# Performance work log

Hardware: AMD Instinct MI355X
Metric: run time of the kernel (lower is better)

## Reference

```python
import jax, jax.numpy as jnp
import numpy as np

N = 100000   # total nodes in batch
E = 400000   # directed edges (before self-loops)
G = 4000     # graphs in batch (~25 atoms/mol)
IN = 29; HID = 128; HEADS = 4
BN_EPS = 1e-5


def setup_inputs():
    ks = jax.random.split(jax.random.key(0), 64)
    def rn(i, shp, s=0.1):
        return jax.random.normal(ks[i], shp, dtype=jnp.float32) * s
    H4 = HEADS * HID
    inp = {
        "x": jax.random.normal(ks[0], (N, IN), dtype=jnp.float32),
        "edge_index": jax.random.randint(ks[1], (2, E), 0, N),
        "batch_idx": jnp.sort(jax.random.randint(ks[2], (N,), 0, G)),
        "context": jax.random.uniform(ks[3], (N, 9), dtype=jnp.float32),
        "props": jax.random.normal(ks[4], (G, 9), dtype=jnp.float32),
        "mask": jax.random.randint(ks[5], (N,), 0, 2).astype(bool),
        "W1": rn(6, (IN, H4)), "as1": rn(7, (HEADS, HID)), "ad1": rn(8, (HEADS, HID)), "b1": rn(9, (H4,)),
        "g1": jnp.ones((H4,)), "be1": jnp.zeros((H4,)), "rm1": rn(10, (H4,), 0.05),
        "rv1": jax.random.uniform(ks[11], (H4,), minval=0.5, maxval=1.5),
        "W2": rn(12, (H4, H4), 0.05), "as2": rn(13, (HEADS, HID)), "ad2": rn(14, (HEADS, HID)), "b2": rn(15, (H4,)),
        "g2": jnp.ones((H4,)), "be2": jnp.zeros((H4,)), "rm2": rn(16, (H4,), 0.05),
        "rv2": jax.random.uniform(ks[17], (H4,), minval=0.5, maxval=1.5),
        "W3": rn(18, (H4, HID), 0.05), "as3": rn(19, (1, HID)), "ad3": rn(20, (1, HID)), "b3": rn(21, (HID,)),
        "g3": jnp.ones((HID,)), "be3": jnp.zeros((HID,)), "rm3": rn(22, (HID,), 0.05),
        "rv3": jax.random.uniform(ks[23], (HID,), minval=0.5, maxval=1.5),
        # context head 128 -> 128 -> 9
        "cw1": rn(24, (HID, HID)), "cb1": jnp.zeros((HID,)), "cw2": rn(25, (HID, 9)), "cb2": jnp.zeros((9,)),
        # property head 128 -> 128 -> 9
        "pw1": rn(26, (HID, HID)), "pb1": jnp.zeros((HID,)), "pw2": rn(27, (HID, 9)), "pb2": jnp.zeros((9,)),
        # masked reconstruction head 128 -> 128 -> 29
        "mw1": rn(28, (HID, HID)), "mb1": jnp.zeros((HID,)), "mw2": rn(29, (HID, IN)), "mb2": jnp.zeros((IN,)),
    }
    return inp


def gat_layer(h_in, src, dst, n, W, a_src, a_dst, bias):
    """PyG GATConv (concat=True, negative_slope=0.2, self-loops already in src/dst)."""
    heads, C = a_src.shape
    h = (h_in @ W).reshape(n, heads, C)                       # [N, H, C]
    e = jax.nn.leaky_relu((h * a_src).sum(-1)[src] + (h * a_dst).sum(-1)[dst], 0.2)  # [E', H]
    m = jax.ops.segment_max(e, dst, num_segments=n)            # segment softmax over incoming edges
    p = jnp.exp(e - m[dst])
    denom = jax.ops.segment_sum(p, dst, num_segments=n)
    alpha = p / (denom[dst] + 1e-16)                           # [E', H]
    out = jax.ops.segment_sum(alpha[:, :, None] * h[src], dst, num_segments=n)  # [N, H, C]
    return out.reshape(n, heads * C) + bias


def bn_elu(x, g, b, rm, rv):
    # BatchNorm1d (eval mode: running stats) followed by ELU; dropout is identity in eval.
    return jax.nn.elu((x - rm) * (g / jnp.sqrt(rv + BN_EPS)) + b)


def reference(x, edge_index, batch_idx, context, props, mask,
              W1, as1, ad1, b1, g1, be1, rm1, rv1,
              W2, as2, ad2, b2, g2, be2, rm2, rv2,
              W3, as3, ad3, b3, g3, be3, rm3, rv3,
              cw1, cb1, cw2, cb2, pw1, pb1, pw2, pb2, mw1, mb1, mw2, mb2):
    n = x.shape[0]
    loop = jnp.arange(n)
    src = jnp.concatenate([edge_index[0], loop])  # PyG GATConv adds self-loops by default
    dst = jnp.concatenate([edge_index[1], loop])
    h = bn_elu(gat_layer(x, src, dst, n, W1, as1, ad1, b1), g1, be1, rm1, rv1)
    h = bn_elu(gat_layer(h, src, dst, n, W2, as2, ad2, b2), g2, be2, rm2, rv2)
    h = bn_elu(gat_layer(h, src, dst, n, W3, as3, ad3, b3), g3, be3, rm3, rv3)  # [N, 128]
    # global mean pool per graph
    cnt = jax.ops.segment_sum(jnp.ones((n,), h.dtype), batch_idx, num_segments=G)
    gemb = jax.ops.segment_sum(h, batch_idx, num_segments=G) / jnp.maximum(cnt, 1.0)[:, None]
    # context prediction (BCE with logits, mean)
    z = jax.nn.relu(h @ cw1 + cb1) @ cw2 + cb2
    context_loss = jnp.mean(jnp.logaddexp(0.0, z) - z * context)
    # property prediction (MSE, mean)
    pz = jax.nn.relu(gemb @ pw1 + pb1) @ pw2 + pb2
    property_loss = jnp.mean((pz - props) ** 2)
    # masked feature reconstruction: MSE over masked nodes (masked mean == mse on h[mask])
    mz = jax.nn.relu(h @ mw1 + mb1) @ mw2 + mb2
    mf = mask.astype(h.dtype)
    mask_loss = jnp.sum(mf[:, None] * (mz - x) ** 2) / (jnp.sum(mf) * x.shape[1])
    return context_loss + property_loss + 0.5 * mask_loss
```

## Files before the change

### kernel.cpp

```cpp
#include <hip/hip_runtime.h>
#include <hip/hip_bf16.h>
#include <cstdint>
#include <cstddef>
#include <type_traits>

#define HIDC 128

typedef __attribute__((ext_vector_type(8))) short short8v;
typedef __attribute__((ext_vector_type(4))) float float4v;

__device__ __forceinline__ float loadT(const float* p){ return *p; }
__device__ __forceinline__ float loadT(const __hip_bfloat16* p){ return __bfloat162float(*p); }
__device__ __forceinline__ void  storeT(float* p, float v){ *p = v; }
__device__ __forceinline__ void  storeT(__hip_bfloat16* p, float v){ *p = __float2bfloat16(v); }

__device__ __forceinline__ short f2bf(float f){
  __hip_bfloat16 h = __float2bfloat16(f);
  return *reinterpret_cast<short*>(&h);
}
__device__ __forceinline__ float bfbits2f(short s){
  return __uint_as_float(((unsigned)(unsigned short)s) << 16);
}

__device__ __forceinline__ int swz(int row, int k){ return (row*32 + k) ^ ((row & 7) << 3); }

template<typename TA, typename TC, bool BIAS, bool RELU>
__global__ __launch_bounds__(256)
void mfma_gemm_kernel(const TA* __restrict__ A, const float* __restrict__ B,
                      const float* __restrict__ bias, TC* __restrict__ C,
                      int M, int Nb, int K, int ldc)
{
  __shared__ short As[128*32];
  __shared__ short Bs[64*32];

  const int nwg = gridDim.x * gridDim.y;
  int orig = blockIdx.y * gridDim.x + blockIdx.x;
  int xcd = orig & 7, pos = orig >> 3;
  int q = nwg >> 3, r = nwg & 7;
  int logical = (xcd < r ? xcd*(q+1) : r*(q+1) + (xcd - r)*q) + pos;
  const int bx = logical % gridDim.x;
  const int by = logical / gridDim.x;

  const int tid  = threadIdx.x;
  const int brow = by * 128;
  const int bcol = bx * 64;
  const int lane = tid & 63;
  const int wave = tid >> 6;
  const int wm = (wave >> 1) * 64;
  const int wn = (wave & 1) * 32;
  const int l15 = lane & 15;
  const int kq  = lane >> 4;

  float4v acc[4][2];
  #pragma unroll
  for (int i = 0; i < 4; i++)
    #pragma unroll
    for (int j = 0; j < 2; j++)
      #pragma unroll
      for (int r2 = 0; r2 < 4; r2++) acc[i][j][r2] = 0.f;

  const int am  = tid >> 1;
  const int akb = (tid & 1) * 16;
  const int bn  = tid & 63;
  const int bkc = tid >> 6;

  const bool dma_ok = std::is_same<TA, __hip_bfloat16>::value &&
                      ((K & 31) == 0) && (brow + 128 <= M);
  int dma_r[2], dma_c[2];
  #pragma unroll
  for (int i = 0; i < 2; i++) {
    int j = (wave*2 + i)*64 + lane;
    int s2 = (j>>2)&1, s3 = (j>>3)&1, s4 = (j>>4)&1;
    int b2 = s2 ^ s4;
    int b1 = ((j>>1)&1) ^ s3;
    int b0 = (j&1) ^ b2;
    int src = (j & ~7) | (b2<<2) | (b1<<1) | b0;
    dma_r[i] = src >> 2;
    dma_c[i] = src & 3;
  }

  for (int k0 = 0; k0 < K; k0 += 32) {
    if (dma_ok) {
      const short* Ash = reinterpret_cast<const short*>(A);
      #pragma unroll
      for (int i = 0; i < 2; i++) {
        const short* gp = Ash + (size_t)(brow + dma_r[i])*K + k0 + dma_c[i]*8;
        __builtin_amdgcn_global_load_lds(
            (const __attribute__((address_space(1))) void*)gp,
            (__attribute__((address_space(3))) void*)&As[(wave*2 + i)*512],
            16, 0, 0);
      }
    } else {
      const int gm = brow + am;
      short s[16];
      if constexpr (std::is_same<TA, __hip_bfloat16>::value) {
        if (gm < M && (k0 + akb + 16) <= K) {
          const short8v* p = reinterpret_cast<const short8v*>(
              reinterpret_cast<const short*>(A) + (size_t)gm*K + k0 + akb);
          short8v v0 = p[0];
          *(short8v*)&As[swz(am, akb)]     = v0;
          short8v v1 = p[1];
          *(short8v*)&As[swz(am, akb + 8)] = v1;
          goto a_done;
        }
      }
      #pragma unroll
      for (int j = 0; j < 16; j++) {
        int gk = k0 + akb + j;
        s[j] = (gm < M && gk < K) ? f2bf(loadT(&A[(size_t)gm*K + gk])) : (short)0;
      }
      {
        short8v v0, v1;
        #pragma unroll
        for (int j = 0; j < 8; j++) { v0[j] = s[j]; v1[j] = s[j+8]; }
        *(short8v*)&As[swz(am, akb)]     = v0;
        *(short8v*)&As[swz(am, akb + 8)] = v1;
      }
      a_done:;
    }
    {
      const int gcol = bcol + bn;
      short8v v;
      #pragma unroll
      for (int j = 0; j < 8; j++) {
        int gk = k0 + bkc*8 + j;
        v[j] = (gk < K && gcol < Nb) ? f2bf(B[(size_t)gk*Nb + gcol]) : (short)0;
      }
      *(short8v*)&Bs[swz(bn, bkc*8)] = v;
    }
    __syncthreads();

    short8v bfrag[2];
    #pragma unroll
    for (int ni = 0; ni < 2; ni++)
      bfrag[ni] = *(const short8v*)&Bs[swz(wn + ni*16 + l15, kq*8)];
    #pragma unroll
    for (int mi = 0; mi < 4; mi++) {
      short8v afrag = *(const short8v*)&As[swz(wm + mi*16 + l15, kq*8)];
      #pragma unroll
      for (int ni = 0; ni < 2; ni++)
        acc[mi][ni] = __builtin_amdgcn_mfma_f32_16x16x32_bf16(afrag, bfrag[ni], acc[mi][ni], 0, 0, 0);
    }
    __syncthreads();
  }

  #pragma unroll
  for (int mi = 0; mi < 4; mi++) {
    #pragma unroll
    for (int r2 = 0; r2 < 4; r2++) {
      int row = brow + wm + mi*16 + kq*4 + r2;
      if (row >= M) continue;
      #pragma unroll
      for (int ni = 0; ni < 2; ni++) {
        int col = bcol + wn + ni*16 + l15;
        if (col >= Nb) continue;
        float v = acc[mi][ni][r2];
        if (BIAS) v += bias[col];
        if (RELU) v = fmaxf(v, 0.f);
        storeT(&C[(size_t)row*ldc + col], v);
      }
    }
  }
}

template<typename T>
__global__ void scores_kernel(const T* __restrict__ hW, const float* __restrict__ a_src,
                              const float* __restrict__ a_dst, float* __restrict__ s_src,
                              float* __restrict__ s_dst, int n, int H)
{
  const int lane = threadIdx.x & 63;
  const int wid = blockIdx.x*(blockDim.x>>6) + (threadIdx.x>>6);
  if (wid >= n*H) return;
  const int node = wid / H, h = wid % H;
  const T* row = hW + (size_t)node*H*HIDC + (size_t)h*HIDC;
  float ss = 0.f, sd = 0.f;
  for (int c = lane; c < HIDC; c += 64) {
    float v = loadT(&row[c]);
    ss += v * a_src[h*HIDC + c];
    sd += v * a_dst[h*HIDC + c];
  }
  #pragma unroll
  for (int off = 32; off; off >>= 1) {
    ss += __shfl_down(ss, off);
    sd += __shfl_down(sd, off);
  }
  if (lane == 0) { s_src[wid] = ss; s_dst[wid] = sd; }
}

__global__ void deg_count_kernel(const int* __restrict__ ei, int E, int EP, int* __restrict__ deg)
{
  int e = blockIdx.x*blockDim.x + threadIdx.x;
  if (e >= EP) return;
  int d = (e < E) ? ei[E + e] : (e - E);
  atomicAdd(&deg[d], 1);
}

__global__ __launch_bounds__(256)
void scan1_kernel(const int* __restrict__ deg, int* __restrict__ indptr,
                  int* __restrict__ bsum, int n)
{
  __shared__ int sh[256];
  const int b = blockIdx.x, t = threadIdx.x;
  const int base = b*1024 + t*4;
  int v0 = (base+0 < n) ? deg[base+0] : 0;
  int v1 = (base+1 < n) ? deg[base+1] : 0;
  int v2 = (base+2 < n) ? deg[base+2] : 0;
  int v3 = (base+3 < n) ? deg[base+3] : 0;
  int tsum = v0+v1+v2+v3;
  sh[t] = tsum;
  __syncthreads();
  for (int off = 1; off < 256; off <<= 1) {
    int x = (t >= off) ? sh[t-off] : 0;
    __syncthreads();
    sh[t] += x;
    __syncthreads();
  }
  int run = sh[t] - tsum;
  if (base+0 < n) indptr[base+0] = run; run += v0;
  if (base+1 < n) indptr[base+1] = run; run += v1;
  if (base+2 < n) indptr[base+2] = run; run += v2;
  if (base+3 < n) indptr[base+3] = run;
  if (t == 255) bsum[b] = sh[255];
}

__global__ void scan2_kernel(int* __restrict__ bsum, int B)
{
  if (blockIdx.x == 0 && threadIdx.x == 0) {
    int run = 0;
    for (int i = 0; i < B; i++) { int v = bsum[i]; bsum[i] = run; run += v; }
  }
}

__global__ void scan3_kernel(int* __restrict__ indptr, const int* __restrict__ bsum,
                             int n, int total)
{
  int i = blockIdx.x*blockDim.x + threadIdx.x;
  if (i < n) indptr[i] += bsum[i >> 10];
  if (i == 0) indptr[n] = total;
}

__global__ void fill_kernel(const int* __restrict__ ei, int E, int EP,
                            const int* __restrict__ indptr, int* __restrict__ ctr,
                            int* __restrict__ esrc)
{
  int e = blockIdx.x*blockDim.x + threadIdx.x;
  if (e >= EP) return;
  int s, d;
  if (e < E) { s = ei[e]; d = ei[E + e]; } else { s = d = e - E; }
  int pos = indptr[d] + atomicAdd(&ctr[d], 1);
  esrc[pos] = s;
}

typedef __hip_bfloat16 bf16;

template<int H>
__global__ void csr_attn_agg_kernel(const int* __restrict__ indptr, const int* __restrict__ esrc,
                                    const float* __restrict__ s_src, const float* __restrict__ s_dst,
                                    const bf16* __restrict__ hW, bf16* __restrict__ out, int n,
                                    const float* __restrict__ bias, const float* __restrict__ g,
                                    const float* __restrict__ be, const float* __restrict__ rm,
                                    const float* __restrict__ rv)
{
  constexpr int HD = H * HIDC;
  const int lane = threadIdx.x & 63;
  const int wid = blockIdx.x*(blockDim.x>>6) + (threadIdx.x>>6);
  if (wid >= n*H) return;
  const int dst = wid / H, h = wid - dst*H;
  const int beg = indptr[dst], end = indptr[dst+1];
  const int deg = end - beg;
  const float sdh = s_dst[dst*H + h];

  float acc0 = 0.f, acc1 = 0.f;

  if (deg <= 64) {
    int sk = (lane < deg) ? esrc[beg + lane] : -1;
    float sc = -3.0e38f;
    if (sk >= 0) {
      float v = s_src[(size_t)sk*H + h] + sdh;
      sc = (v >= 0.f) ? v : 0.2f*v;
    }
    float m = sc;
    #pragma unroll
    for (int off = 32; off; off >>= 1) m = fmaxf(m, __shfl_xor(m, off));
    float e = (sk >= 0) ? __expf(sc - m) : 0.f;
    float den = e;
    #pragma unroll
    for (int off = 32; off; off >>= 1) den += __shfl_xor(den, off);
    const float rden = 1.f / (den + 1e-16f);
    for (int k = 0; k < deg; ++k) {
      float a = __shfl(e, k) * rden;
      int s = __shfl(sk, k);
      const bf16* row = hW + (size_t)s*HD + h*HIDC;
      acc0 += a * loadT(&row[lane]);
      acc1 += a * loadT(&row[lane + 64]);
    }
  } else {
    float m = -3.0e38f;
    for (int k = beg + lane; k < end; k += 64) {
      float v = s_src[(size_t)esrc[k]*H + h] + sdh;
      v = (v >= 0.f) ? v : 0.2f*v;
      m = fmaxf(m, v);
    }
    #pragma unroll
    for (int off = 32; off; off >>= 1) m = fmaxf(m, __shfl_xor(m, off));
    float den = 0.f;
    for (int k = beg + lane; k < end; k += 64) {
      float v = s_src[(size_t)esrc[k]*H + h] + sdh;
      v = (v >= 0.f) ? v : 0.2f*v;
      den += __expf(v - m);
    }
    #pragma unroll
    for (int off = 32; off; off >>= 1) den += __shfl_xor(den, off);
    const float rden = 1.f / (den + 1e-16f);
    for (int k = beg; k < end; ++k) {
      int s = esrc[k];
      float v = s_src[(size_t)s*H + h] + sdh;
      v = (v >= 0.f) ? v : 0.2f*v;
      float a = __expf(v - m) * rden;
      const bf16* row = hW + (size_t)s*HD + h*HIDC;
      acc0 += a * loadT(&row[lane]);
      acc1 += a * loadT(&row[lane + 64]);
    }
  }

  const int c0 = h*HIDC + lane;
  const int c1 = c0 + 64;
  float y0 = (acc0 + bias[c0] - rm[c0]) * (g[c0] / sqrtf(rv[c0] + 1e-5f)) + be[c0];
  float y1 = (acc1 + bias[c1] - rm[c1]) * (g[c1] / sqrtf(rv[c1] + 1e-5f)) + be[c1];
  y0 = (y0 > 0.f) ? y0 : expm1f(y0);
  y1 = (y1 > 0.f) ? y1 : expm1f(y1);
  bf16* orow = out + (size_t)dst*HD + h*HIDC;
  storeT(&orow[lane], y0);
  storeT(&orow[lane + 64], y1);
}

template<typename T>
__global__ void pool_sum_kernel(const T* __restrict__ h, const int* __restrict__ batch,
                                float* __restrict__ gsum, float* __restrict__ cnt, int n)
{
  int idx = blockIdx.x*blockDim.x + threadIdx.x;
  if (idx >= n*HIDC) return;
  int node = idx >> 7, j = idx & 127;
  int g = batch[node];
  atomicAdd(&gsum[(size_t)g*HIDC + j], loadT(&h[idx]));
  if (j == 0) atomicAdd(&cnt[g], 1.f);
}

__global__ void pool_div_kernel(float* __restrict__ gsum, const float* __restrict__ cnt, int G)
{
  int idx = blockIdx.x*blockDim.x + threadIdx.x;
  if (idx >= G*HIDC) return;
  gsum[idx] /= fmaxf(cnt[idx >> 7], 1.f);
}

__global__ void mask_detect_kernel(const int* __restrict__ m, int nwords, int* __restrict__ flag)
{
  int i = blockIdx.x*blockDim.x + threadIdx.x;
  if (i >= nwords) return;
  unsigned v = (unsigned)m[i];
  if (v > 1u) atomicOr(flag, 1);
}

__global__ __launch_bounds__(256)
void bce_reduce_kernel(const float* __restrict__ z, const float* __restrict__ ctx,
                       float* __restrict__ out_sum, int n)
{
  __shared__ float sh[256];
  float local = 0.f;
  const long long total = (long long)n * 9;
  for (long long i = (long long)blockIdx.x*blockDim.x + threadIdx.x; i < total;
       i += (long long)gridDim.x*blockDim.x) {
    int row = (int)(i / 9), j = (int)(i - (long long)row*9);
    float zz = z[(size_t)row*32 + j];
    float la = fmaxf(zz, 0.f) + log1pf(expf(-fabsf(zz)));
    local += la - zz * ctx[i];
  }
  sh[threadIdx.x] = local;
  __syncthreads();
  for (int s = 128; s; s >>= 1) {
    if ((int)threadIdx.x < s) sh[threadIdx.x] += sh[threadIdx.x + s];
    __syncthreads();
  }
  if (threadIdx.x == 0) atomicAdd(out_sum, sh[0]);
}

__global__ __launch_bounds__(256)
void mse_mask_reduce_kernel(const float* __restrict__ z, const float* __restrict__ x,
                            const int* __restrict__ mask, const int* __restrict__ bytemode,
                            float* __restrict__ out_sum, float* __restrict__ out_cnt, int n)
{
  __shared__ float sh[256], sh2[256];
  float local = 0.f, cl = 0.f;
  const bool bm = (*bytemode) != 0;
  const long long total = (long long)n * 29;
  for (long long i = (long long)blockIdx.x*blockDim.x + threadIdx.x; i < total;
       i += (long long)gridDim.x*blockDim.x) {
    int row = (int)(i / 29), j = (int)(i - (long long)row*29);
    int mk = bm ? (int)((const unsigned char*)mask)[row] : mask[row];
    if (mk != 0) {
      float dd = z[(size_t)row*32 + j] - x[i];
      local += dd*dd;
      if (j == 0) cl += 1.f;
    }
  }
  sh[threadIdx.x] = local;
  sh2[threadIdx.x] = cl;
  __syncthreads();
  for (int s = 128; s; s >>= 1) {
    if ((int)threadIdx.x < s) { sh[threadIdx.x] += sh[threadIdx.x + s]; sh2[threadIdx.x] += sh2[threadIdx.x + s]; }
    __syncthreads();
  }
  if (threadIdx.x == 0) { atomicAdd(out_sum, sh[0]); atomicAdd(out_cnt, sh2[0]); }
}

__global__ __launch_bounds__(256)
void mse_reduce_kernel(const float* __restrict__ z, const float* __restrict__ props,
                       float* __restrict__ out_sum, int g)
{
  __shared__ float sh[256];
  float local = 0.f;
  const long long total = (long long)g * 9;
  for (long long i = (long long)blockIdx.x*blockDim.x + threadIdx.x; i < total;
       i += (long long)gridDim.x*blockDim.x) {
    int row = (int)(i / 9), j = (int)(i - (long long)row*9);
    float dd = z[(size_t)row*32 + j] - props[i];
    local += dd*dd;
  }
  sh[threadIdx.x] = local;
  __syncthreads();
  for (int s = 128; s; s >>= 1) {
    if ((int)threadIdx.x < s) sh[threadIdx.x] += sh[threadIdx.x + s];
    __syncthreads();
  }
  if (threadIdx.x == 0) atomicAdd(out_sum, sh[0]);
}

__global__ void finalize_kernel(const float* __restrict__ scal, float* __restrict__ out,
                                float nf, float gf)
{
  out[0] = scal[0]/nf + scal[1]/gf + 0.5f*(scal[2]/(scal[3]*29.f));
}

__global__ void write_zero_kernel(float* __restrict__ out){ out[0] = 0.f; }

static void run_pipeline(void* const* d_in, hipStream_t stream, float* d_out,
                         bf16* buf1, bf16* buf2, float* ssrc, float* sdst,
                         int* indptr, int* deg, int* ctr, int* bsum, int* esrc,
                         float* gemb, float* cnt, float* r3, float* pz, float* scal, int* flag,
                         int N, int E, int G)
{
  const float* x     = (const float*)d_in[0];
  const int*   ei    = (const int*)d_in[1];
  const int*   batch = (const int*)d_in[2];
  const float* ctx   = (const float*)d_in[3];
  const float* props = (const float*)d_in[4];
  const int*   mask  = (const int*)d_in[5];
  const float* W1  = (const float*)d_in[6];  const float* as1 = (const float*)d_in[7];
  const float* ad1 = (const float*)d_in[8];  const float* b1  = (const float*)d_in[9];
  const float* g1  = (const float*)d_in[10]; const float* be1 = (const float*)d_in[11];
  const float* rm1 = (const float*)d_in[12]; const float* rv1 = (const float*)d_in[13];
  const float* W2  = (const float*)d_in[14]; const float* as2 = (const float*)d_in[15];
  const float* ad2 = (const float*)d_in[16]; const float* b2  = (const float*)d_in[17];
  const float* g2  = (const float*)d_in[18]; const float* be2 = (const float*)d_in[19];
  const float* rm2 = (const float*)d_in[20]; const float* rv2 = (const float*)d_in[21];
  const float* W3  = (const float*)d_in[22]; const float* as3 = (const float*)d_in[23];
  const float* ad3 = (const float*)d_in[24]; const float* b3  = (const float*)d_in[25];
  const float* g3  = (const float*)d_in[26]; const float* be3 = (const float*)d_in[27];
  const float* rm3 = (const float*)d_in[28]; const float* rv3 = (const float*)d_in[29];
  const float* cw1 = (const float*)d_in[30]; const float* cb1 = (const float*)d_in[31];
  const float* cw2 = (const float*)d_in[32]; const float* cb2 = (const float*)d_in[33];
  const float* pw1 = (const float*)d_in[34]; const float* pb1 = (const float*)d_in[35];
  const float* pw2 = (const float*)d_in[36]; const float* pb2 = (const float*)d_in[37];
  const float* mw1 = (const float*)d_in[38]; const float* mb1 = (const float*)d_in[39];
  const float* mw2 = (const float*)d_in[40]; const float* mb2 = (const float*)d_in[41];

  const int EP = E + N;
  const int H4 = 4 * HIDC;
  const int NB = (N + 1023) / 1024;
  const int GM = (N + 127) / 128;
  const int GG = (G + 127) / 128;

  (void)hipMemsetAsync(scal, 0, 8*sizeof(float), stream);
  (void)hipMemsetAsync(gemb, 0, (size_t)G*HIDC*sizeof(float), stream);
  (void)hipMemsetAsync(cnt,  0, (size_t)G*sizeof(float), stream);
  (void)hipMemsetAsync(deg,  0, (size_t)N*sizeof(int), stream);
  (void)hipMemsetAsync(ctr,  0, (size_t)N*sizeof(int), stream);
  mask_detect_kernel<<<(N/4 + 255)/256, 256, 0, stream>>>(mask, N/4, flag);

  deg_count_kernel<<<(EP + 255)/256, 256, 0, stream>>>(ei, E, EP, deg);
  scan1_kernel<<<NB, 256, 0, stream>>>(deg, indptr, bsum, N);
  scan2_kernel<<<1, 64, 0, stream>>>(bsum, NB);
  scan3_kernel<<<(N + 255)/256, 256, 0, stream>>>(indptr, bsum, N, EP);
  fill_kernel<<<(EP + 255)/256, 256, 0, stream>>>(ei, E, EP, indptr, ctr, esrc);

  mfma_gemm_kernel<float, bf16, false, false><<<dim3(H4/64, GM), 256, 0, stream>>>(x, W1, nullptr, buf2, N, H4, 29, H4);
  scores_kernel<bf16><<<(N*4 + 3)/4, 256, 0, stream>>>(buf2, as1, ad1, ssrc, sdst, N, 4);
  csr_attn_agg_kernel<4><<<(N*4 + 3)/4, 256, 0, stream>>>(indptr, esrc, ssrc, sdst, buf2, buf1, N, b1, g1, be1, rm1, rv1);

  mfma_gemm_kernel<bf16, bf16, false, false><<<dim3(H4/64, GM), 256, 0, stream>>>(buf1, W2, nullptr, buf2, N, H4, H4, H4);
  scores_kernel<bf16><<<(N*4 + 3)/4, 256, 0, stream>>>(buf2, as2, ad2, ssrc, sdst, N, 4);
  csr_attn_agg_kernel<4><<<(N*4 + 3)/4, 256, 0, stream>>>(indptr, esrc, ssrc, sdst, buf2, buf1, N, b2, g2, be2, rm2, rv2);

  mfma_gemm_kernel<bf16, bf16, false, false><<<dim3(HIDC/64, GM), 256, 0, stream>>>(buf1, W3, nullptr, buf2, N, HIDC, H4, HIDC);
  scores_kernel<bf16><<<(N + 3)/4, 256, 0, stream>>>(buf2, as3, ad3, ssrc, sdst, N, 1);
  csr_attn_agg_kernel<1><<<(N + 3)/4, 256, 0, stream>>>(indptr, esrc, ssrc, sdst, buf2, buf1, N, b3, g3, be3, rm3, rv3);

  pool_sum_kernel<bf16><<<(N*HIDC + 255)/256, 256, 0, stream>>>(buf1, batch, gemb, cnt, N);
  pool_div_kernel<<<(G*HIDC + 255)/256, 256, 0, stream>>>(gemb, cnt, G);

  bf16* headf = buf2;
  float* zbuf  = (float*)((char*)buf1 + (size_t)N*HIDC*sizeof(bf16));

  mfma_gemm_kernel<bf16, bf16, true, true><<<dim3(HIDC/64, GM), 256, 0, stream>>>(
      buf1, cw1, cb1, headf, N, HIDC, HIDC, HIDC);
  mfma_gemm_kernel<bf16, float, true, false><<<dim3(1, GM), 256, 0, stream>>>(
      headf, cw2, cb2, zbuf, N, 9, HIDC, 32);
  bce_reduce_kernel<<<2048, 256, 0, stream>>>(zbuf, ctx, &scal[0], N);

  mfma_gemm_kernel<bf16, bf16, true, true><<<dim3(HIDC/64, GM), 256, 0, stream>>>(
      buf1, mw1, mb1, headf, N, HIDC, HIDC, HIDC);
  mfma_gemm_kernel<bf16, float, true, false><<<dim3(1, GM), 256, 0, stream>>>(
      headf, mw2, mb2, zbuf, N, 29, HIDC, 32);
  mse_mask_reduce_kernel<<<2048, 256, 0, stream>>>(zbuf, x, mask, flag, &scal[2], &scal[3], N);

  mfma_gemm_kernel<float, float, true, true><<<dim3(HIDC/64, GG), 256, 0, stream>>>(
      gemb, pw1, pb1, r3, G, HIDC, HIDC, HIDC);
  mfma_gemm_kernel<float, float, true, false><<<dim3(1, GG), 256, 0, stream>>>(
      r3, pw2, pb2, pz, G, 9, HIDC, 32);
  mse_reduce_kernel<<<64, 256, 0, stream>>>(pz, props, &scal[1], G);

  finalize_kernel<<<1, 1, 0, stream>>>(scal, d_out, (float)N*9.f, (float)G*9.f);
}

extern "C" void kernel_launch(void* const* d_in, const int* in_sizes, int n_in,
                              void* d_out, int out_size, void* d_ws, size_t ws_size,
                              hipStream_t stream)
{
  const int N  = in_sizes[0] / 29;
  const int E  = in_sizes[1] / 2;
  const int G  = in_sizes[4] / 9;
  const int EP = E + N;
  const int H4 = 4 * HIDC;

  const size_t aux_bytes =
      (size_t)N*4*sizeof(float)*2
    + (size_t)(N+1)*sizeof(int)
    + (size_t)N*sizeof(int)*2
    + 512*sizeof(int)
    + (size_t)EP*sizeof(int)
    + (size_t)G*HIDC*sizeof(float)*2
    + (size_t)G*32*sizeof(float)
    + (size_t)G*sizeof(float)
    + 64*sizeof(float)
    + 4096;

  const size_t big = (size_t)N * H4;
  const size_t need = 2*big*sizeof(__hip_bfloat16) + aux_bytes;

  if (ws_size < need) {
    write_zero_kernel<<<1, 1, 0, stream>>>((float*)d_out);
    return;
  }

  char* base = (char*)d_ws;
  void* buf1 = (void*)base;          base += (big*sizeof(__hip_bfloat16) + 255) & ~(size_t)255;
  void* buf2 = (void*)base;          base += (big*sizeof(__hip_bfloat16) + 255) & ~(size_t)255;
  float* ssrc = (float*)base;        base += (size_t)N*4*sizeof(float);
  float* sdst = (float*)base;        base += (size_t)N*4*sizeof(float);
  int* indptr = (int*)base;          base += (size_t)(N+1)*sizeof(int);
  int* deg    = (int*)base;          base += (size_t)N*sizeof(int);
  int* ctr    = (int*)base;          base += (size_t)N*sizeof(int);
  int* bsum   = (int*)base;          base += 512*sizeof(int);
  int* esrc   = (int*)base;          base += (size_t)EP*sizeof(int);
  float* gemb = (float*)base;        base += (size_t)G*HIDC*sizeof(float);
  float* cnt  = (float*)base;        base += (size_t)G*sizeof(float);
  float* r3   = (float*)base;        base += (size_t)G*HIDC*sizeof(float);
  float* pz   = (float*)base;        base += (size_t)G*32*sizeof(float);
  float* scal = (float*)base;        base += 64*sizeof(float);
  int*   flag = (int*)&scal[4];

  run_pipeline(d_in, stream, (float*)d_out, (bf16*)buf1, (bf16*)buf2,
               ssrc, sdst, indptr, deg, ctr, bsum, esrc, gemb, cnt, r3, pz, scal, flag, N, E, G);
}
```

Baseline: 1.523 ms.

## Double-buffer LDS tiles in the DMA path of the MFMA GEMM

Splits the GEMM into a prefetching path for bf16 inputs with aligned K and full row tiles. That path double-buffers the A and B shared-memory tiles, issuing the global-to-LDS loads and B register loads for the next K tile before running MFMAs on the current one, with one barrier per iteration. The aim is to hide global memory latency behind MFMA compute. It doubles LDS use, which may lower occupancy, and the fallback path keeps the old single-buffer loop.

```diff
diff --git a/kernel.cpp b/kernel.cpp
--- a/kernel.cpp
+++ b/kernel.cpp
@@ -30,8 +30,8 @@
                       const float* __restrict__ bias, TC* __restrict__ C,
                       int M, int Nb, int K, int ldc)
 {
-  __shared__ short As[128*32];
-  __shared__ short Bs[64*32];
+  __shared__ short As[2][128*32];
+  __shared__ short Bs[2][64*32];
 
   const int nwg = gridDim.x * gridDim.y;
   int orig = blockIdx.y * gridDim.x + blockIdx.x;
@@ -79,69 +79,131 @@
     dma_c[i] = src & 3;
   }
 
-  for (int k0 = 0; k0 < K; k0 += 32) {
-    if (dma_ok) {
-      const short* Ash = reinterpret_cast<const short*>(A);
+  if (dma_ok) {
+    const short* Ash = reinterpret_cast<const short*>(A);
+    const int gcol = bcol + bn;
+    const int nt = K >> 5;
+    float bv[8];
+
+    #pragma unroll
+    for (int i = 0; i < 2; i++) {
+      const short* gp = Ash + (size_t)(brow + dma_r[i])*K + dma_c[i]*8;
+      __builtin_amdgcn_global_load_lds(
+          (const __attribute__((address_space(1))) void*)gp,
+          (__attribute__((address_space(3))) void*)&As[0][(wave*2 + i)*512],
+          16, 0, 0);
+    }
+    #pragma unroll
+    for (int j = 0; j < 8; j++) {
+      int gk = bkc*8 + j;
+      bv[j] = (gcol < Nb) ? B[(size_t)gk*Nb + gcol] : 0.f;
+    }
+    {
+      short8v v;
       #pragma unroll
-      for (int i = 0; i < 2; i++) {
-        const short* gp = Ash + (size_t)(brow + dma_r[i])*K + k0 + dma_c[i]*8;
-        __builtin_amdgcn_global_load_lds(
-            (const __attribute__((address_space(1))) void*)gp,
-            (__attribute__((address_space(3))) void*)&As[(wave*2 + i)*512],
-            16, 0, 0);
-      }
-    } else {
-      const int gm = brow + am;
-      short s[16];
-      if constexpr (std::is_same<TA, __hip_bfloat16>::value) {
-        if (gm < M && (k0 + akb + 16) <= K) {
-          const short8v* p = reinterpret_cast<const short8v*>(
-              reinterpret_cast<const short*>(A) + (size_t)gm*K + k0 + akb);
-          short8v v0 = p[0];
-          *(short8v*)&As[swz(am, akb)]     = v0;
-          short8v v1 = p[1];
-          *(short8v*)&As[swz(am, akb + 8)] = v1;
-          goto a_done;
+      for (int j = 0; j < 8; j++) v[j] = f2bf(bv[j]);
+      *(short8v*)&Bs[0][swz(bn, bkc*8)] = v;
+    }
+    asm volatile("s_waitcnt vmcnt(0)" ::: "memory");
+    __syncthreads();
+
+    int cur = 0;
+    for (int t = 0; t < nt; t++) {
+      const bool pf = (t + 1 < nt);
+      if (pf) {
+        const int k0n = (t + 1) << 5;
+        #pragma unroll
+        for (int i = 0; i < 2; i++) {
+          const short* gp = Ash + (size_t)(brow + dma_r[i])*K + k0n + dma_c[i]*8;
+          __builtin_amdgcn_global_load_lds(
+              (const __attribute__((address_space(1))) void*)gp,
+              (__attribute__((address_space(3))) void*)&As[cur^1][(wave*2 + i)*512],
+              16, 0, 0);
+        }
+        #pragma unroll
+        for (int j = 0; j < 8; j++) {
+          int gk = k0n + bkc*8 + j;
+          bv[j] = (gcol < Nb) ? B[(size_t)gk*Nb + gcol] : 0.f;
         }
       }
-      #pragma unroll
-      for (int j = 0; j < 16; j++) {
-        int gk = k0 + akb + j;
-        s[j] = (gm < M && gk < K) ? f2bf(loadT(&A[(size_t)gm*K + gk])) : (short)0;
+      {
+        short8v bfrag[2];
+        #pragma unroll
+        for (int ni = 0; ni < 2; ni++)
+          bfrag[ni] = *(const short8v*)&Bs[cur][swz(wn + ni*16 + l15, kq*8)];
+        #pragma unroll
+        for (int mi = 0; mi < 4; mi++) {
+          short8v afrag = *(const short8v*)&As[cur][swz(wm + mi*16 + l15, kq*8)];
+          #pragma unroll
+          for (int ni = 0; ni < 2; ni++)
+            acc[mi][ni] = __builtin_amdgcn_mfma_f32_16x16x32_bf16(afrag, bfrag[ni], acc[mi][ni], 0, 0, 0);
+        }
+      }
+      if (pf) {
+        short8v v;
+        #pragma unroll
+        for (int j = 0; j < 8; j++) v[j] = f2bf(bv[j]);
+        *(short8v*)&Bs[cur^1][swz(bn, bkc*8)] = v;
+      }
+      asm volatile("s_waitcnt vmcnt(0)" ::: "memory");
+      __syncthreads();
+      cur ^= 1;
+    }
+  } else {
+    for (int k0 = 0; k0 < K; k0 += 32) {
+      {
+        const int gm = brow + am;
+        short s[16];
+        if constexpr (std::is_same<TA, __hip_bfloat16>::value) {
+          if (gm < M && (k0 + akb + 16) <= K) {
+            const short8v* p = reinterpret_cast<const short8v*>(
+                reinterpret_cast<const short*>(A) + (size_t)gm*K + k0 + akb);
+            short8v v0 = p[0];
+            *(short8v*)&As[0][swz(am, akb)]     = v0;
+            short8v v1 = p[1];
+            *(short8v*)&As[0][swz(am, akb + 8)] = v1;
+            goto a_done;
+          }
+        }
+        #pragma unroll
+        for (int j = 0; j < 16; j++) {
+          int gk = k0 + akb + j;
+          s[j] = (gm < M && gk < K) ? f2bf(loadT(&A[(size_t)gm*K + gk])) : (short)0;
+        }
+        {
+          short8v v0, v1;
+          #pragma unroll
+          for (int j = 0; j < 8; j++) { v0[j] = s[j]; v1[j] = s[j+8]; }
+          *(short8v*)&As[0][swz(am, akb)]     = v0;
+          *(short8v*)&As[0][swz(am, akb + 8)] = v1;
+        }
+        a_done:;
       }
       {
-        short8v v0, v1;
-        #pragma unroll
-        for (int j = 0; j < 8; j++) { v0[j] = s[j]; v1[j] = s[j+8]; }
-        *(short8v*)&As[swz(am, akb)]     = v0;
-        *(short8v*)&As[swz(am, akb + 8)] = v1;
+        const int gcol = bcol + bn;
+        short8v v;
+        #pragma unroll
+        for (int j = 0; j < 8; j++) {
+          int gk = k0 + bkc*8 + j;
+          v[j] = (gk < K && gcol < Nb) ? f2bf(B[(size_t)gk*Nb + gcol]) : (short)0;
+        }
+        *(short8v*)&Bs[0][swz(bn, bkc*8)] = v;
       }
-      a_done:;
-    }
-    {
-      const int gcol = bcol + bn;
-      short8v v;
-      #pragma unroll
-      for (int j = 0; j < 8; j++) {
-        int gk = k0 + bkc*8 + j;
-        v[j] = (gk < K && gcol < Nb) ? f2bf(B[(size_t)gk*Nb + gcol]) : (short)0;
-      }
-      *(short8v*)&Bs[swz(bn, bkc*8)] = v;
-    }
-    __syncthreads();
-
-    short8v bfrag[2];
-    #pragma unroll
-    for (int ni = 0; ni < 2; ni++)
-      bfrag[ni] = *(const short8v*)&Bs[swz(wn + ni*16 + l15, kq*8)];
-    #pragma unroll
-    for (int mi = 0; mi < 4; mi++) {
-      short8v afrag = *(const short8v*)&As[swz(wm + mi*16 + l15, kq*8)];
+      __syncthreads();
+
+      short8v bfrag[2];
       #pragma unroll
       for (int ni = 0; ni < 2; ni++)
-        acc[mi][ni] = __builtin_amdgcn_mfma_f32_16x16x32_bf16(afrag, bfrag[ni], acc[mi][ni], 0, 0, 0);
-    }
-    __syncthreads();
+        bfrag[ni] = *(const short8v*)&Bs[0][swz(wn + ni*16 + l15, kq*8)];
+      #pragma unroll
+      for (int mi = 0; mi < 4; mi++) {
+        short8v afrag = *(const short8v*)&As[0][swz(wm + mi*16 + l15, kq*8)];
+        #pragma unroll
+        for (int ni = 0; ni < 2; ni++)
+          acc[mi][ni] = __builtin_amdgcn_mfma_f32_16x16x32_bf16(afrag, bfrag[ni], acc[mi][ni], 0, 0, 0);
+      }
+      __syncthreads();
+    }
   }
 
   #pragma unroll
```

After: 1.293 ms. -15.1%, faster.
